# Optimization experiments

Measured on AMD Instinct MI355X. Metric: run time of the kernel, lower is better.

The kernel has to match this reference:

```python
import jax, jax.numpy as jnp
import numpy as np

B, S, D_IN, D, H = 2, 2048, 512, 1024, 16
HD = D // H


def _linear_params(key, d_in, d_out):
    kw, kb = jax.random.split(key)
    bound = 1.0 / np.sqrt(d_in)
    W = jax.random.uniform(kw, (d_in, d_out), jnp.float32, -bound, bound)
    b = jax.random.uniform(kb, (d_out,), jnp.float32, -bound, bound)
    return W, b


def setup_inputs() -> dict:
    key = jax.random.key(0)
    keys = jax.random.split(key, 8)
    x = jax.random.normal(keys[0], (B, S, D_IN), jnp.float32)
    We, be = _linear_params(keys[1], D_IN, D)
    Wq, bq = _linear_params(keys[2], D, D)
    Wk, bk = _linear_params(keys[3], D, D)
    Wv, bv = _linear_params(keys[4], D, D)
    W0, b0 = _linear_params(keys[5], D, D)
    W1, b1 = _linear_params(keys[6], D, D)
    W2, b2 = _linear_params(keys[7], D, D)
    return {"x": x, "We": We, "be": be, "Wq": Wq, "bq": bq, "Wk": Wk, "bk": bk,
            "Wv": Wv, "bv": bv, "W0": W0, "b0": b0, "W1": W1, "b1": b1, "W2": W2, "b2": b2}


def reference(x, We, be, Wq, bq, Wk, bk, Wv, bv, W0, b0, W1, b1, W2, b2):
    # embedding
    e = x @ We + be                                   # [B,S,D]
    q = (e @ Wq + bq).reshape(B, S, H, HD)            # [B,S,H,hd]
    k = (e @ Wk + bk).reshape(B, S, H, HD)
    v = (e @ Wv + bv).reshape(B, S, H, HD)
    scale = 1.0 / jnp.sqrt(jnp.float32(HD))
    scores = jnp.einsum('bqhd,bkhd->bhqk', q, k) * scale
    attn = jax.nn.softmax(scores, axis=-1)            # [B,H,S,S]
    ctx = jnp.einsum('bhqk,bkhd->bqhd', attn, v).reshape(B, S, D)
    mha = e + (ctx @ W0 + b0)                         # residual
    ffn = jax.nn.relu(mha @ W1 + b1) @ W2 + b2
    return mha + ffn
```

## Files before the change

kernel.cpp:

```cpp
#include <hip/hip_runtime.h>

typedef unsigned short u16;
typedef __bf16 bf16x8 __attribute__((ext_vector_type(8)));
typedef float f32x4 __attribute__((ext_vector_type(4)));

__device__ __forceinline__ float bf2f(u16 u) {
  return __builtin_bit_cast(float, (unsigned)u << 16);
}
__device__ __forceinline__ u16 f2bf(float f) {
  unsigned u = __builtin_bit_cast(unsigned, f);
  u += 0x7FFFu + ((u >> 16) & 1u);
  return (u16)(u >> 16);
}
__device__ __forceinline__ unsigned pk2(float a, float b) {
  return (unsigned)f2bf(a) | ((unsigned)f2bf(b) << 16);
}
__device__ __forceinline__ unsigned pk2t(float a, float b) {
  return __builtin_amdgcn_perm(__builtin_bit_cast(unsigned, b),
                               __builtin_bit_cast(unsigned, a), 0x07060302u);
}
__device__ __forceinline__ f32x4 mfma16(bf16x8 a, bf16x8 b, f32x4 c) {
  return __builtin_amdgcn_mfma_f32_16x16x32_bf16(a, b, c, 0, 0, 0);
}
__device__ __forceinline__ void async_cp16(const u16* g, u16* l) {
  __builtin_amdgcn_global_load_lds((const __attribute__((address_space(1))) void*)g,
                                   (__attribute__((address_space(3))) void*)l, 16, 0, 0);
}
#define S_BARRIER() asm volatile("s_barrier" ::: "memory")

__global__ __launch_bounds__(256) void cast_f32_bf16(const float* __restrict__ in,
                                                     u16* __restrict__ out, int n) {
  int idx = (blockIdx.x * 256 + threadIdx.x) * 4;
  if (idx < n) {
    float4 f = *(const float4*)&in[idx];
    ushort4 o;
    o.x = f2bf(f.x); o.y = f2bf(f.y); o.z = f2bf(f.z); o.w = f2bf(f.w);
    *(ushort4*)&out[idx] = o;
  }
}

__global__ __launch_bounds__(256) void biascat(const float* __restrict__ bq,
                                               const float* __restrict__ bk,
                                               const float* __restrict__ bv,
                                               float* __restrict__ o) {
  int i = blockIdx.x * 256 + threadIdx.x;
  if (i < 3072)
    o[i] = i < 1024 ? bq[i] : (i < 2048 ? bk[i - 1024] : bv[i - 2048]);
}

#define TSP 72
__global__ __launch_bounds__(256) void transpose_weights(
    const float* __restrict__ We, const float* __restrict__ Wq,
    const float* __restrict__ Wk, const float* __restrict__ Wv,
    const float* __restrict__ W0, const float* __restrict__ W1,
    const float* __restrict__ W2, u16* Wet, u16* qkvWt, u16* W0t, u16* W1t,
    u16* W2t) {
  const int z = blockIdx.z;
  const float* in;
  u16* out;
  int out_rs = 1024;
  if (z == 0) { if (blockIdx.y >= 8) return; in = We; out = Wet; out_rs = 512; }
  else if (z == 1) { in = Wq; out = qkvWt; }
  else if (z == 2) { in = Wk; out = qkvWt + 1048576; }
  else if (z == 3) { in = Wv; out = qkvWt + 2097152; }
  else if (z == 4) { in = W0; out = W0t; }
  else if (z == 5) { in = W1; out = W1t; }
  else { in = W2; out = W2t; }
  __shared__ alignas(16) u16 T[64][TSP];
  const int tid = threadIdx.x;
  const int r0 = blockIdx.y * 64, c0 = blockIdx.x * 64;
#pragma unroll
  for (int it = 0; it < 4; ++it) {
    int vi = it * 256 + tid;
    int i = vi >> 4, j4 = (vi & 15) * 4;
    float4 f = *(const float4*)&in[(size_t)(r0 + i) * 1024 + c0 + j4];
    T[i][j4 + 0] = f2bf(f.x);
    T[i][j4 + 1] = f2bf(f.y);
    T[i][j4 + 2] = f2bf(f.z);
    T[i][j4 + 3] = f2bf(f.w);
  }
  __syncthreads();
#pragma unroll
  for (int it = 0; it < 2; ++it) {
    int vi = it * 256 + tid;
    int i = vi >> 3, j8 = (vi & 7) * 8;
    bf16x8 v;
#pragma unroll
    for (int u = 0; u < 8; ++u) ((u16*)&v)[u] = T[j8 + u][i];
    *(bf16x8*)&out[(size_t)(c0 + i) * out_rs + r0 + j8] = v;
  }
}

__global__ __launch_bounds__(256, 2) void gemm_mfma(
    const u16* __restrict__ A, const u16* __restrict__ Bt,
    const float* __restrict__ bias, const u16* __restrict__ res,
    void* __restrict__ Cout, int M, int N, int K, int relu, int f32out) {
  __shared__ alignas(16) u16 As[2][128 * 64];
  __shared__ alignas(16) u16 Bs[2][128 * 64];
  const int tid = threadIdx.x;
  const int wave = tid >> 6, lane = tid & 63;
  const int quad = lane >> 4, l16 = lane & 15;
  const int ib = blockIdx.x;
  const int by = (ib & 7) * 4 + ((ib >> 3) & 3);
  const int bx = ib >> 5;
  const int m0 = by * 128, n0 = bx * 128;
  const int wm = (wave & 1) * 64, wn = (wave >> 1) * 64;

  f32x4 acc[4][4];
#pragma unroll
  for (int i = 0; i < 4; ++i)
#pragma unroll
    for (int j = 0; j < 4; ++j) acc[i][j] = (f32x4){0.f, 0.f, 0.f, 0.f};

  const int srow = lane >> 3;
  const int schunk = (lane & 7) ^ (srow & 7);
  const u16* Ag = A + (size_t)(m0 + wave * 32 + srow) * K + schunk * 8;
  const u16* Bg = Bt + (size_t)(n0 + wave * 32 + srow) * K + schunk * 8;
  u16* AsW0 = &As[0][wave * 32 * 64];
  u16* BsW0 = &Bs[0][wave * 32 * 64];
  u16* AsW1 = &As[1][wave * 32 * 64];
  u16* BsW1 = &Bs[1][wave * 32 * 64];

#define GEMM_ISSUE(ab, bb, k)                                     \
  {                                                               \
    _Pragma("unroll") for (int i = 0; i < 4; ++i)                 \
        async_cp16(Ag + (k) + (size_t)i * 8 * K, (ab) + i * 512); \
    _Pragma("unroll") for (int i = 0; i < 4; ++i)                 \
        async_cp16(Bg + (k) + (size_t)i * 8 * K, (bb) + i * 512); \
  }

  GEMM_ISSUE(AsW0, BsW0, 0);
  const int T = K >> 6;
  const int swz = (l16 & 7);
  for (int t = 0; t < T; ++t) {
    const int cb = t & 1;
    S_BARRIER();
    const int kn = (t + 1 < T) ? ((t + 1) << 6) : 0;
    if (cb == 0) GEMM_ISSUE(AsW1, BsW1, kn) else GEMM_ISSUE(AsW0, BsW0, kn);
    asm volatile("s_waitcnt vmcnt(8)" ::: "memory");
    S_BARRIER();
#pragma unroll
    for (int kk = 0; kk < 2; ++kk) {
      bf16x8 af[4], bfr[4];
#pragma unroll
      for (int mt = 0; mt < 4; ++mt)
        af[mt] = *(const bf16x8*)&As[cb][(wm + mt * 16 + l16) * 64 +
                                        ((kk * 4 + quad) ^ swz) * 8];
#pragma unroll
      for (int nt = 0; nt < 4; ++nt)
        bfr[nt] = *(const bf16x8*)&Bs[cb][(wn + nt * 16 + l16) * 64 +
                                          ((kk * 4 + quad) ^ swz) * 8];
#pragma unroll
      for (int mt = 0; mt < 4; ++mt)
#pragma unroll
        for (int nt = 0; nt < 4; ++nt)
          acc[mt][nt] = mfma16(af[mt], bfr[nt], acc[mt][nt]);
    }
  }
  asm volatile("s_waitcnt vmcnt(0)" ::: "memory");

#pragma unroll
  for (int nt = 0; nt < 4; ++nt) {
    int col = n0 + wn + nt * 16 + l16;
    float bv = bias[col];
#pragma unroll
    for (int mt = 0; mt < 4; ++mt) {
#pragma unroll
      for (int r = 0; r < 4; ++r) {
        int row = m0 + wm + mt * 16 + quad * 4 + r;
        float v = acc[mt][nt][r] + bv;
        if (res) v += bf2f(res[(size_t)row * N + col]);
        if (relu) v = fmaxf(v, 0.f);
        if (f32out)
          ((float*)Cout)[(size_t)row * N + col] = v;
        else
          ((u16*)Cout)[(size_t)row * N + col] = f2bf(v);
      }
    }
  }
}

__global__ __launch_bounds__(256, 2) void attn_kernel(
    const u16* __restrict__ QKV, const u16* __restrict__ Vt,
    u16* __restrict__ O) {
  __shared__ alignas(16) u16 Ks[2][64 * 64];
  __shared__ alignas(16) u16 Vs[2][64 * 64];
  __shared__ alignas(16) u16 Ps[4][32 * 72];
  const int tid = threadIdx.x;
  const int wave = tid >> 6, lane = tid & 63;
  const int quad = lane >> 4, l16 = lane & 15;
  const int ib = blockIdx.x;
  const int bh = ib & 31, b = bh >> 4, h = bh & 15;
  const int q0 = (ib >> 5) * 128 + wave * 32;

  bf16x8 qf[2][2];
#pragma unroll
  for (int qt = 0; qt < 2; ++qt) {
    const size_t qoff = (size_t)(b * 2048 + q0 + qt * 16 + l16) * 3072 + h * 64;
#pragma unroll
    for (int kk = 0; kk < 2; ++kk) {
      bf16x8 raw = *(const bf16x8*)&QKV[qoff + kk * 32 + quad * 8];
#pragma unroll
      for (int u = 0; u < 8; ++u)
        ((u16*)&raw)[u] = f2bf(0.125f * bf2f(((u16*)&raw)[u]));
      qf[qt][kk] = raw;
    }
  }
  bf16x8 ones;
#pragma unroll
  for (int u = 0; u < 8; ++u) ((u16*)&ones)[u] = 0x3F80;

  f32x4 o[4][2];
  f32x4 l_acc[2] = {(f32x4){0.f, 0.f, 0.f, 0.f}, (f32x4){0.f, 0.f, 0.f, 0.f}};
#pragma unroll
  for (int mt = 0; mt < 4; ++mt)
#pragma unroll
    for (int qt = 0; qt < 2; ++qt) o[mt][qt] = (f32x4){0.f, 0.f, 0.f, 0.f};

  const int srow = lane >> 3;
  const int schunk = (lane & 7) ^ (srow & 7);
  const u16* Kg = QKV + (size_t)(b * 2048 + wave * 16 + srow) * 3072 + 1024 +
                  h * 64 + schunk * 8;
  const u16* Vg = Vt + (size_t)((b * 16 + h) * 64 + wave * 16 + srow) * 2048 +
                  schunk * 8;
  u16* KsW0 = &Ks[0][(wave * 16) * 64];
  u16* VsW0 = &Vs[0][(wave * 16) * 64];
  u16* KsW1 = &Ks[1][(wave * 16) * 64];
  u16* VsW1 = &Vs[1][(wave * 16) * 64];

#define ATTN_ISSUE(kb, vb, kt)                                \
  {                                                           \
    async_cp16(Kg + (size_t)(kt) * 3072, (kb));               \
    async_cp16(Kg + (size_t)((kt) + 8) * 3072, (kb) + 512);   \
    async_cp16(Vg + (kt), (vb));                              \
    async_cp16(Vg + (kt) + (size_t)8 * 2048, (vb) + 512);     \
  }

  ATTN_ISSUE(KsW0, VsW0, 0);
  const int swz = (l16 & 7);
  u16* PsW = &Ps[wave][0];
  for (int t = 0; t < 32; ++t) {
    const int cb = t & 1;
    S_BARRIER();
    const int ktn = (t + 1 < 32) ? ((t + 1) * 64) : 0;
    if (cb == 0) ATTN_ISSUE(KsW1, VsW1, ktn) else ATTN_ISSUE(KsW0, VsW0, ktn);
    asm volatile("s_waitcnt vmcnt(4)" ::: "memory");
    S_BARRIER();

    f32x4 st[4][2];
#pragma unroll
    for (int km = 0; km < 4; ++km)
#pragma unroll
      for (int qt = 0; qt < 2; ++qt) st[km][qt] = (f32x4){0.f, 0.f, 0.f, 0.f};
#pragma unroll
    for (int kk = 0; kk < 2; ++kk)
#pragma unroll
      for (int km = 0; km < 4; ++km) {
        bf16x8 kf = *(const bf16x8*)&Ks[cb][(km * 16 + l16) * 64 +
                                           ((kk * 4 + quad) ^ swz) * 8];
        st[km][0] = mfma16(kf, qf[0][kk], st[km][0]);
        st[km][1] = mfma16(kf, qf[1][kk], st[km][1]);
      }

#pragma unroll
    for (int qt = 0; qt < 2; ++qt)
#pragma unroll
      for (int km = 0; km < 4; ++km) {
        float e0 = __expf(st[km][qt][0]), e1 = __expf(st[km][qt][1]);
        float e2 = __expf(st[km][qt][2]), e3 = __expf(st[km][qt][3]);
        uint2 pk;
        pk.x = pk2t(e0, e1);
        pk.y = pk2t(e2, e3);
        *(uint2*)&PsW[(qt * 16 + l16) * 72 + km * 16 + quad * 4] = pk;
      }
    asm volatile("s_waitcnt lgkmcnt(0)" ::: "memory");

#pragma unroll
    for (int kk2 = 0; kk2 < 2; ++kk2) {
      bf16x8 pf0 = *(const bf16x8*)&PsW[l16 * 72 + kk2 * 32 + quad * 8];
      bf16x8 pf1 = *(const bf16x8*)&PsW[(16 + l16) * 72 + kk2 * 32 + quad * 8];
      l_acc[0] = mfma16(ones, pf0, l_acc[0]);
      l_acc[1] = mfma16(ones, pf1, l_acc[1]);
#pragma unroll
      for (int mt = 0; mt < 4; ++mt) {
        bf16x8 vf = *(const bf16x8*)&Vs[cb][(mt * 16 + l16) * 64 +
                                           ((kk2 * 4 + quad) ^ swz) * 8];
        o[mt][0] = mfma16(vf, pf0, o[mt][0]);
        o[mt][1] = mfma16(vf, pf1, o[mt][1]);
      }
    }
  }
  asm volatile("s_waitcnt vmcnt(0)" ::: "memory");

#pragma unroll
  for (int qt = 0; qt < 2; ++qt) {
    float inv = 1.f / l_acc[qt][0];
    size_t base = (size_t)(b * 2048 + q0 + qt * 16 + l16) * 1024 + h * 64;
#pragma unroll
    for (int mt = 0; mt < 4; ++mt) {
      uint2 pk;
      pk.x = pk2(o[mt][qt][0] * inv, o[mt][qt][1] * inv);
      pk.y = pk2(o[mt][qt][2] * inv, o[mt][qt][3] * inv);
      *(uint2*)&O[base + mt * 16 + quad * 4] = pk;
    }
  }
}

__global__ __launch_bounds__(256) void transpose_v(const u16* __restrict__ QKV,
                                                   u16* __restrict__ vt) {
  const int bh = blockIdx.y;
  const int b = bh >> 4, h = bh & 15;
  const int s0 = blockIdx.x * 64;
  const u16* in = QKV + (size_t)b * 2048 * 3072 + 2048 + h * 64;
  u16* out = vt + (size_t)bh * 131072;
  __shared__ alignas(16) u16 T[64][TSP];
  const int tid = threadIdx.x;
#pragma unroll
  for (int it = 0; it < 2; ++it) {
    int vi = it * 256 + tid;
    int i = vi >> 3, j8 = (vi & 7) * 8;
    *(bf16x8*)&T[i][j8] = *(const bf16x8*)&in[(size_t)(s0 + i) * 3072 + j8];
  }
  __syncthreads();
#pragma unroll
  for (int it = 0; it < 2; ++it) {
    int vi = it * 256 + tid;
    int i = vi >> 3, j8 = (vi & 7) * 8;
    bf16x8 vv;
#pragma unroll
    for (int u = 0; u < 8; ++u) ((u16*)&vv)[u] = T[j8 + u][i];
    *(bf16x8*)&out[(size_t)i * 2048 + s0 + j8] = vv;
  }
}

extern "C" void kernel_launch(void* const* d_in, const int* in_sizes, int n_in,
                              void* d_out, int out_size, void* d_ws,
                              size_t ws_size, hipStream_t stream) {
  const float* x = (const float*)d_in[0];
  const float* We = (const float*)d_in[1];
  const float* be = (const float*)d_in[2];
  const float* Wq = (const float*)d_in[3];
  const float* bq = (const float*)d_in[4];
  const float* Wk = (const float*)d_in[5];
  const float* bk = (const float*)d_in[6];
  const float* Wv = (const float*)d_in[7];
  const float* bv = (const float*)d_in[8];
  const float* W0 = (const float*)d_in[9];
  const float* b0 = (const float*)d_in[10];
  const float* W1 = (const float*)d_in[11];
  const float* b1 = (const float*)d_in[12];
  const float* W2 = (const float*)d_in[13];
  const float* b2 = (const float*)d_in[14];

  u16* ws = (u16*)d_ws;
  u16* xb = ws;
  u16* Wet = xb + 2097152;
  u16* qkvWt = Wet + 524288;
  u16* ctx = ws;
  u16* W0t = qkvWt + 3145728;
  u16* W1t = W0t + 1048576;
  u16* W2t = W1t + 1048576;
  float* biasqkv = (float*)(W2t + 1048576);
  u16* e = W2t + 1048576 + 6144;
  u16* qkv = e + 4194304;
  u16* vtb = qkv + 12582912;
  u16* mha = qkv;
  u16* h1 = e;

  cast_f32_bf16<<<2048, 256, 0, stream>>>(x, xb, 4096 * 512);
  transpose_weights<<<dim3(16, 16, 7), 256, 0, stream>>>(
      We, Wq, Wk, Wv, W0, W1, W2, Wet, qkvWt, W0t, W1t, W2t);
  biascat<<<12, 256, 0, stream>>>(bq, bk, bv, biasqkv);

  gemm_mfma<<<256, 256, 0, stream>>>(xb, Wet, be, nullptr, e, 4096, 1024, 512,
                                     0, 0);
  gemm_mfma<<<768, 256, 0, stream>>>(e, qkvWt, biasqkv, nullptr, qkv, 4096,
                                     3072, 1024, 0, 0);
  transpose_v<<<dim3(32, 32), 256, 0, stream>>>(qkv, vtb);
  attn_kernel<<<512, 256, 0, stream>>>(qkv, vtb, ctx);
  gemm_mfma<<<256, 256, 0, stream>>>(ctx, W0t, b0, e, mha, 4096, 1024, 1024, 0,
                                     0);
  gemm_mfma<<<256, 256, 0, stream>>>(mha, W1t, b1, nullptr, h1, 4096, 1024,
                                     1024, 1, 0);
  gemm_mfma<<<256, 256, 0, stream>>>(h1, W2t, b2, mha, d_out, 4096, 1024, 1024,
                                     0, 1);
}
```

Before: 302.6 us.

## Pre-pack weights in MFMA fragment layout and load B directly to registers

The weight transpose kernel now writes weights in a packed 16-row by 8-element fragment layout, so the GEMM can load B operands straight from global memory into registers. Only A is staged through LDS, with a smaller 64x128 tile. This doubles the grid size and raises the occupancy hint to 3 blocks per SM. It cuts LDS traffic and footprint, at the cost of more redundant global loads of B across M-tiles and more register pressure from double-buffered B fragments.

```diff
diff --git a/kernel.cpp b/kernel.cpp
--- a/kernel.cpp
+++ b/kernel.cpp
@@ -58,8 +58,8 @@
   const int z = blockIdx.z;
   const float* in;
   u16* out;
-  int out_rs = 1024;
-  if (z == 0) { if (blockIdx.y >= 8) return; in = We; out = Wet; out_rs = 512; }
+  int Kc = 128;
+  if (z == 0) { if (blockIdx.y >= 8) return; in = We; out = Wet; Kc = 64; }
   else if (z == 1) { in = Wq; out = qkvWt; }
   else if (z == 2) { in = Wk; out = qkvWt + 1048576; }
   else if (z == 3) { in = Wv; out = qkvWt + 2097152; }
@@ -83,88 +83,100 @@
 #pragma unroll
   for (int it = 0; it < 2; ++it) {
     int vi = it * 256 + tid;
-    int i = vi >> 3, j8 = (vi & 7) * 8;
+    int n_loc = vi >> 3, kcl = vi & 7;
     bf16x8 v;
 #pragma unroll
-    for (int u = 0; u < 8; ++u) ((u16*)&v)[u] = T[j8 + u][i];
-    *(bf16x8*)&out[(size_t)(c0 + i) * out_rs + r0 + j8] = v;
-  }
-}
-
-__global__ __launch_bounds__(256, 2) void gemm_mfma(
-    const u16* __restrict__ A, const u16* __restrict__ Bt,
+    for (int u = 0; u < 8; ++u) ((u16*)&v)[u] = T[kcl * 8 + u][n_loc];
+    int nt16 = (c0 + n_loc) >> 4;
+    int kc = (r0 >> 3) + kcl;
+    *(bf16x8*)&out[(((size_t)nt16 * Kc + kc) * 16 + (n_loc & 15)) * 8] = v;
+  }
+}
+
+__global__ __launch_bounds__(256, 3) void gemm_mfma(
+    const u16* __restrict__ A, const u16* __restrict__ Bp,
     const float* __restrict__ bias, const u16* __restrict__ res,
     void* __restrict__ Cout, int M, int N, int K, int relu, int f32out) {
-  __shared__ alignas(16) u16 As[2][128 * 64];
-  __shared__ alignas(16) u16 Bs[2][128 * 64];
+  __shared__ alignas(16) u16 As[2][64 * 64];
   const int tid = threadIdx.x;
   const int wave = tid >> 6, lane = tid & 63;
   const int quad = lane >> 4, l16 = lane & 15;
   const int ib = blockIdx.x;
-  const int by = (ib & 7) * 4 + ((ib >> 3) & 3);
-  const int bx = ib >> 5;
-  const int m0 = by * 128, n0 = bx * 128;
-  const int wm = (wave & 1) * 64, wn = (wave >> 1) * 64;
-
-  f32x4 acc[4][4];
-#pragma unroll
-  for (int i = 0; i < 4; ++i)
+  const int by = (ib & 7) * 8 + ((ib >> 3) & 7);
+  const int bx = ib >> 6;
+  const int m0 = by * 64, n0 = bx * 128;
+  const int wm = (wave & 1) * 32, wn16 = (wave >> 1) * 4;
+  const int Kc = K >> 3;
+
+  f32x4 acc[2][4];
+#pragma unroll
+  for (int i = 0; i < 2; ++i)
 #pragma unroll
     for (int j = 0; j < 4; ++j) acc[i][j] = (f32x4){0.f, 0.f, 0.f, 0.f};
 
   const int srow = lane >> 3;
   const int schunk = (lane & 7) ^ (srow & 7);
-  const u16* Ag = A + (size_t)(m0 + wave * 32 + srow) * K + schunk * 8;
-  const u16* Bg = Bt + (size_t)(n0 + wave * 32 + srow) * K + schunk * 8;
-  u16* AsW0 = &As[0][wave * 32 * 64];
-  u16* BsW0 = &Bs[0][wave * 32 * 64];
-  u16* AsW1 = &As[1][wave * 32 * 64];
-  u16* BsW1 = &Bs[1][wave * 32 * 64];
-
-#define GEMM_ISSUE(ab, bb, k)                                     \
-  {                                                               \
-    _Pragma("unroll") for (int i = 0; i < 4; ++i)                 \
-        async_cp16(Ag + (k) + (size_t)i * 8 * K, (ab) + i * 512); \
-    _Pragma("unroll") for (int i = 0; i < 4; ++i)                 \
-        async_cp16(Bg + (k) + (size_t)i * 8 * K, (bb) + i * 512); \
-  }
-
-  GEMM_ISSUE(AsW0, BsW0, 0);
+  const u16* Ag = A + (size_t)(m0 + wave * 16 + srow) * K + schunk * 8;
+  u16* AsW0 = &As[0][wave * 16 * 64];
+  u16* AsW1 = &As[1][wave * 16 * 64];
+  const u16* Bpw = Bp + ((size_t)(n0 / 16 + wn16) * Kc) * 128 + l16 * 8;
+
+  bf16x8 bA[2][4], bB[2][4];
+
+#define ISSUE_A(ab, k)                                    \
+  {                                                       \
+    async_cp16(Ag + (k), (ab));                           \
+    async_cp16(Ag + (k) + (size_t)8 * K, (ab) + 512);     \
+  }
+#define LOAD_B(bt, k0c)                                                      \
+  {                                                                          \
+    _Pragma("unroll") for (int kk = 0; kk < 2; ++kk)                         \
+        _Pragma("unroll") for (int nt = 0; nt < 4; ++nt)                     \
+            bt[kk][nt] = *(const bf16x8*)&Bpw[((size_t)nt * Kc +             \
+                                              (k0c) + kk * 4 + quad) * 128]; \
+  }
+#define COMPUTE(cb, bt)                                                      \
+  {                                                                          \
+    _Pragma("unroll") for (int kk = 0; kk < 2; ++kk) {                       \
+      bf16x8 af[2];                                                          \
+      _Pragma("unroll") for (int mt = 0; mt < 2; ++mt)                       \
+          af[mt] = *(const bf16x8*)&As[cb][(wm + mt * 16 + l16) * 64 +       \
+                                           ((kk * 4 + quad) ^ swz) * 8];     \
+      _Pragma("unroll") for (int mt = 0; mt < 2; ++mt)                       \
+          _Pragma("unroll") for (int nt = 0; nt < 4; ++nt)                   \
+              acc[mt][nt] = mfma16(af[mt], bt[kk][nt], acc[mt][nt]);         \
+    }                                                                        \
+  }
+
+  ISSUE_A(AsW0, 0);
+  LOAD_B(bA, 0);
   const int T = K >> 6;
   const int swz = (l16 & 7);
   for (int t = 0; t < T; ++t) {
-    const int cb = t & 1;
     S_BARRIER();
     const int kn = (t + 1 < T) ? ((t + 1) << 6) : 0;
-    if (cb == 0) GEMM_ISSUE(AsW1, BsW1, kn) else GEMM_ISSUE(AsW0, BsW0, kn);
-    asm volatile("s_waitcnt vmcnt(8)" ::: "memory");
-    S_BARRIER();
-#pragma unroll
-    for (int kk = 0; kk < 2; ++kk) {
-      bf16x8 af[4], bfr[4];
-#pragma unroll
-      for (int mt = 0; mt < 4; ++mt)
-        af[mt] = *(const bf16x8*)&As[cb][(wm + mt * 16 + l16) * 64 +
-                                        ((kk * 4 + quad) ^ swz) * 8];
-#pragma unroll
-      for (int nt = 0; nt < 4; ++nt)
-        bfr[nt] = *(const bf16x8*)&Bs[cb][(wn + nt * 16 + l16) * 64 +
-                                          ((kk * 4 + quad) ^ swz) * 8];
-#pragma unroll
-      for (int mt = 0; mt < 4; ++mt)
-#pragma unroll
-        for (int nt = 0; nt < 4; ++nt)
-          acc[mt][nt] = mfma16(af[mt], bfr[nt], acc[mt][nt]);
+    if ((t & 1) == 0) {
+      ISSUE_A(AsW1, kn);
+      LOAD_B(bB, kn >> 3);
+      asm volatile("s_waitcnt vmcnt(10)" ::: "memory");
+      S_BARRIER();
+      COMPUTE(0, bA);
+    } else {
+      ISSUE_A(AsW0, kn);
+      LOAD_B(bA, kn >> 3);
+      asm volatile("s_waitcnt vmcnt(10)" ::: "memory");
+      S_BARRIER();
+      COMPUTE(1, bB);
     }
   }
   asm volatile("s_waitcnt vmcnt(0)" ::: "memory");
 
 #pragma unroll
   for (int nt = 0; nt < 4; ++nt) {
-    int col = n0 + wn + nt * 16 + l16;
+    int col = n0 + wn16 * 16 + nt * 16 + l16;
     float bv = bias[col];
 #pragma unroll
-    for (int mt = 0; mt < 4; ++mt) {
+    for (int mt = 0; mt < 2; ++mt) {
 #pragma unroll
       for (int r = 0; r < 4; ++r) {
         int row = m0 + wm + mt * 16 + quad * 4 + r;
@@ -372,16 +384,16 @@
       We, Wq, Wk, Wv, W0, W1, W2, Wet, qkvWt, W0t, W1t, W2t);
   biascat<<<12, 256, 0, stream>>>(bq, bk, bv, biasqkv);
 
-  gemm_mfma<<<256, 256, 0, stream>>>(xb, Wet, be, nullptr, e, 4096, 1024, 512,
+  gemm_mfma<<<512, 256, 0, stream>>>(xb, Wet, be, nullptr, e, 4096, 1024, 512,
                                      0, 0);
-  gemm_mfma<<<768, 256, 0, stream>>>(e, qkvWt, biasqkv, nullptr, qkv, 4096,
-                                     3072, 1024, 0, 0);
+  gemm_mfma<<<1536, 256, 0, stream>>>(e, qkvWt, biasqkv, nullptr, qkv, 4096,
+                                      3072, 1024, 0, 0);
   transpose_v<<<dim3(32, 32), 256, 0, stream>>>(qkv, vtb);
   attn_kernel<<<512, 256, 0, stream>>>(qkv, vtb, ctx);
-  gemm_mfma<<<256, 256, 0, stream>>>(ctx, W0t, b0, e, mha, 4096, 1024, 1024, 0,
+  gemm_mfma<<<512, 256, 0, stream>>>(ctx, W0t, b0, e, mha, 4096, 1024, 1024, 0,
                                      0);
-  gemm_mfma<<<256, 256, 0, stream>>>(mha, W1t, b1, nullptr, h1, 4096, 1024,
+  gemm_mfma<<<512, 256, 0, stream>>>(mha, W1t, b1, nullptr, h1, 4096, 1024,
                                      1024, 1, 0);
-  gemm_mfma<<<256, 256, 0, stream>>>(h1, W2t, b2, mha, d_out, 4096, 1024, 1024,
+  gemm_mfma<<<512, 256, 0, stream>>>(h1, W2t, b2, mha, d_out, 4096, 1024, 1024,
                                      0, 1);
 }
```

New measurement: 603.8 us. 2x slower.
